# Optimization experiments

Measured on AMD Instinct MI355X. Metric: run time of the kernel, lower is better.

The kernel has to match this reference:

```python
import jax, jax.numpy as jnp
import numpy as np

# Module hyperparameters (match init_kwargs)
OUT_CHANNELS = 64
K = 19          # kernel_size
STRIDE = 5
PAD = 9
UPPER = 2.99
LOWER = -2.99

B = 64
L = 100000


def setup_inputs() -> dict:
    key = jax.random.key(0)
    k1, k2, k3 = jax.random.split(key, 3)
    x = jax.random.normal(k1, (B, 1, L), dtype=jnp.float32)
    # std_conv params: Conv1d(1, out_channels-2, K) -> weight (O-2, 1, K), bias (O-2,)
    W = jax.random.normal(k2, (OUT_CHANNELS - 2, 1, K), dtype=jnp.float32) * (1.0 / np.sqrt(K))
    b = jax.random.normal(k3, (OUT_CHANNELS - 2,), dtype=jnp.float32) * 0.01
    return {"x": x, "W": W, "b": b}


def _conv1d(x, w, stride, pad):
    # x: [B, Cin, L]; w: [Cout, Cin, K]
    return jax.lax.conv_general_dilated(
        x, w, window_strides=(stride,), padding=[(pad, pad)],
        dimension_numbers=("NCH", "OIH", "NCH"))


def reference(x, W, b):
    # Channel 0: windowed mean (non-differentiable / detached)
    mean_w = jnp.full((1, 1, K), 1.0 / K, dtype=x.dtype)
    mean_ch = jax.lax.stop_gradient(_conv1d(x, mean_w, STRIDE, PAD))  # [B,1,L_out]

    # Channel 1: threshold flag per window. any(x>UP) -> +1 ; elif any(x<LOWER) -> -1 ; else 0.
    # any(x > UP) over a window == (window max > UP); same for min. Zero-pad first
    # to match F.pad(..., value=0), then VALID reduce_window.
    xp = jnp.pad(x, ((0, 0), (0, 0), (PAD, PAD)))
    wmax = jax.lax.reduce_window(xp, -jnp.inf, jax.lax.max, (1, 1, K), (1, 1, STRIDE), "VALID")
    wmin = jax.lax.reduce_window(xp, jnp.inf, jax.lax.min, (1, 1, K), (1, 1, STRIDE), "VALID")
    thr_ch = jnp.where(wmax > UPPER, jnp.asarray(1.0, x.dtype),
                       jnp.where(wmin < LOWER, jnp.asarray(-1.0, x.dtype),
                                 jnp.asarray(0.0, x.dtype)))  # [B,1,L_out]
    thr_ch = jax.lax.stop_gradient(thr_ch)

    # Remaining channels: standard (differentiable) conv1d
    std_ch = _conv1d(x, W, STRIDE, PAD) + b[None, :, None]  # [B,O-2,L_out]

    return jnp.concatenate([mean_ch, thr_ch, std_ch], axis=1)  # [B, OUT_CHANNELS, L_out]
```

## Files before the change

### kernel.cpp

```cpp
#include <hip/hip_runtime.h>


#define BATCH       64
#define LIN         100000
#define LOUT        20000
#define KSZ         19
#define STRIDE_     5
#define PAD_        9
#define CSTD        62
#define UPPER_      2.99f
#define LOWER_      (-2.99f)

#define TPB         256
#define POS_PER_BLK 512
#define BPR         ((LOUT + POS_PER_BLK - 1) / POS_PER_BLK)
#define TILE_IN     ((POS_PER_BLK - 1) * STRIDE_ + KSZ)
#define WROW        20

__global__ __launch_bounds__(TPB)
void conv1d_mean_thr_kernel(const float* __restrict__ x,
                            const float* __restrict__ W,
                            const float* __restrict__ bias,
                            float* __restrict__ out)
{
    __shared__ float tile[TILE_IN];
    __shared__ float wsh[CSTD * WROW];
    __shared__ float bsh[CSTD];

    const int tid   = threadIdx.x;
    const int blk   = blockIdx.x;
    const int batch = blk / BPR;
    const int pblk  = blk - batch * BPR;
    const int p0    = pblk * POS_PER_BLK;
    const long tstart = (long)p0 * STRIDE_ - PAD_;

    const float* xrow = x + (size_t)batch * LIN;
    for (int i = tid; i < TILE_IN; i += TPB) {
        long g = tstart + i;
        tile[i] = (g >= 0 && g < LIN) ? xrow[g] : 0.0f;
    }
    for (int i = tid; i < CSTD * WROW; i += TPB) {
        int c = i / WROW, k = i - c * WROW;
        wsh[i] = (k < KSZ) ? W[c * KSZ + k] : 0.0f;
    }
    if (tid < CSTD) bsh[tid] = bias[tid];
    __syncthreads();

    float xv0[KSZ], xv1[KSZ];
    const int l0 = tid * STRIDE_;
    const int l1 = (tid + TPB) * STRIDE_;
#pragma unroll
    for (int k = 0; k < KSZ; ++k) {
        xv0[k] = tile[l0 + k];
        xv1[k] = tile[l1 + k];
    }

    const int pos0 = p0 + tid;
    const int pos1 = pos0 + TPB;
    const bool v0 = (pos0 < LOUT);
    const bool v1 = (pos1 < LOUT);
    float* orow = out + (size_t)batch * 64 * LOUT;

    float s0 = 0.f, s1 = 0.f;
    float mx0 = -INFINITY, mx1 = -INFINITY;
    float mn0 =  INFINITY, mn1 =  INFINITY;
#pragma unroll
    for (int k = 0; k < KSZ; ++k) {
        s0 += xv0[k]; mx0 = fmaxf(mx0, xv0[k]); mn0 = fminf(mn0, xv0[k]);
        s1 += xv1[k]; mx1 = fmaxf(mx1, xv1[k]); mn1 = fminf(mn1, xv1[k]);
    }
    const float inv_k = 1.0f / (float)KSZ;
    float thr0 = (mx0 > UPPER_) ? 1.0f : ((mn0 < LOWER_) ? -1.0f : 0.0f);
    float thr1 = (mx1 > UPPER_) ? 1.0f : ((mn1 < LOWER_) ? -1.0f : 0.0f);
    if (v0) { orow[pos0] = s0 * inv_k; orow[LOUT + pos0] = thr0; }
    if (v1) { orow[pos1] = s1 * inv_k; orow[LOUT + pos1] = thr1; }

    for (int c = 0; c < CSTD; ++c) {
        const float* wr = &wsh[c * WROW];
        float acc0 = 0.f, acc1 = 0.f;
#pragma unroll
        for (int k = 0; k < KSZ; ++k) {
            float wv = wr[k];
            acc0 = fmaf(xv0[k], wv, acc0);
            acc1 = fmaf(xv1[k], wv, acc1);
        }
        const float bv = bsh[c];
        size_t cbase = (size_t)(c + 2) * LOUT;
        if (v0) orow[cbase + pos0] = acc0 + bv;
        if (v1) orow[cbase + pos1] = acc1 + bv;
    }
}

extern "C" void kernel_launch(void* const* d_in, const int* in_sizes, int n_in,
                              void* d_out, int out_size, void* d_ws, size_t ws_size,
                              hipStream_t stream)
{
    const float* x    = (const float*)d_in[0];
    const float* W    = (const float*)d_in[1];
    const float* bias = (const float*)d_in[2];
    float* out        = (float*)d_out;

    dim3 grid(BATCH * BPR);
    dim3 block(TPB);
    conv1d_mean_thr_kernel<<<grid, block, 0, stream>>>(x, W, bias, out);
}
```

Before: 363.0 us.

## Compute four consecutive outputs per thread with vectorized LDS loads and float4 stores

Each thread now handles four adjacent output positions, so it needs one 36-float input window, loaded from shared memory as nine float4 reads, instead of two separate 19-float windows. Results go out as float4 stores per channel, which cuts the number of store instructions on a write-heavy output. Weights and bias are no longer staged in shared memory; they are read directly from global memory, where the wavefront-uniform addresses can use scalar loads. The trade-off is higher register pressure from the wider input window and a more rigid assumption that output rows are divisible by four and 16-byte aligned.

```diff
diff --git a/kernel.cpp b/kernel.cpp
--- a/kernel.cpp
+++ b/kernel.cpp
@@ -1,21 +1,22 @@
 #include <hip/hip_runtime.h>
 
 
-#define BATCH       64
-#define LIN         100000
-#define LOUT        20000
-#define KSZ         19
-#define STRIDE_     5
-#define PAD_        9
-#define CSTD        62
-#define UPPER_      2.99f
-#define LOWER_      (-2.99f)
+#define BATCH   64
+#define LIN     100000
+#define LOUT    20000
+#define KSZ     19
+#define STRIDE_ 5
+#define PAD_    9
+#define CSTD    62
+#define UPPER_  2.99f
+#define LOWER_  (-2.99f)
 
 #define TPB         256
-#define POS_PER_BLK 512
+#define PPT         4
+#define POS_PER_BLK (TPB * PPT)
 #define BPR         ((LOUT + POS_PER_BLK - 1) / POS_PER_BLK)
 #define TILE_IN     ((POS_PER_BLK - 1) * STRIDE_ + KSZ)
-#define WROW        20
+#define TILE_SZ     5136
 
 __global__ __launch_bounds__(TPB)
 void conv1d_mean_thr_kernel(const float* __restrict__ x,
@@ -23,9 +24,7 @@
                             const float* __restrict__ bias,
                             float* __restrict__ out)
 {
-    __shared__ float tile[TILE_IN];
-    __shared__ float wsh[CSTD * WROW];
-    __shared__ float bsh[CSTD];
+    __shared__ float tile[TILE_SZ];
 
     const int tid   = threadIdx.x;
     const int blk   = blockIdx.x;
@@ -35,59 +34,70 @@
     const long tstart = (long)p0 * STRIDE_ - PAD_;
 
     const float* xrow = x + (size_t)batch * LIN;
-    for (int i = tid; i < TILE_IN; i += TPB) {
+    for (int i = tid; i < TILE_SZ; i += TPB) {
         long g = tstart + i;
         tile[i] = (g >= 0 && g < LIN) ? xrow[g] : 0.0f;
     }
-    for (int i = tid; i < CSTD * WROW; i += TPB) {
-        int c = i / WROW, k = i - c * WROW;
-        wsh[i] = (k < KSZ) ? W[c * KSZ + k] : 0.0f;
-    }
-    if (tid < CSTD) bsh[tid] = bias[tid];
     __syncthreads();
 
-    float xv0[KSZ], xv1[KSZ];
-    const int l0 = tid * STRIDE_;
-    const int l1 = (tid + TPB) * STRIDE_;
+    float xw[36];
+    {
+        const float4* t4 = reinterpret_cast<const float4*>(tile);
 #pragma unroll
-    for (int k = 0; k < KSZ; ++k) {
-        xv0[k] = tile[l0 + k];
-        xv1[k] = tile[l1 + k];
+        for (int k = 0; k < 9; ++k) {
+            float4 v = t4[tid * 5 + k];
+            xw[4 * k + 0] = v.x;
+            xw[4 * k + 1] = v.y;
+            xw[4 * k + 2] = v.z;
+            xw[4 * k + 3] = v.w;
+        }
     }
 
-    const int pos0 = p0 + tid;
-    const int pos1 = pos0 + TPB;
-    const bool v0 = (pos0 < LOUT);
-    const bool v1 = (pos1 < LOUT);
-    float* orow = out + (size_t)batch * 64 * LOUT;
+    const int pos0   = p0 + tid * PPT;
+    const bool valid = (pos0 + PPT - 1) < LOUT;
+    float* outp = out + (size_t)batch * 64 * LOUT + pos0;
 
-    float s0 = 0.f, s1 = 0.f;
-    float mx0 = -INFINITY, mx1 = -INFINITY;
-    float mn0 =  INFINITY, mn1 =  INFINITY;
+    {
+        float mean[PPT], thr[PPT];
+        const float inv_k = 1.0f / (float)KSZ;
 #pragma unroll
-    for (int k = 0; k < KSZ; ++k) {
-        s0 += xv0[k]; mx0 = fmaxf(mx0, xv0[k]); mn0 = fminf(mn0, xv0[k]);
-        s1 += xv1[k]; mx1 = fmaxf(mx1, xv1[k]); mn1 = fminf(mn1, xv1[k]);
+        for (int j = 0; j < PPT; ++j) {
+            float s = 0.f, mx = -INFINITY, mn = INFINITY;
+#pragma unroll
+            for (int k = 0; k < KSZ; ++k) {
+                float v = xw[5 * j + k];
+                s += v; mx = fmaxf(mx, v); mn = fminf(mn, v);
+            }
+            mean[j] = s * inv_k;
+            thr[j]  = (mx > UPPER_) ? 1.0f : ((mn < LOWER_) ? -1.0f : 0.0f);
+        }
+        if (valid) {
+            *reinterpret_cast<float4*>(outp) =
+                make_float4(mean[0], mean[1], mean[2], mean[3]);
+            *reinterpret_cast<float4*>(outp + LOUT) =
+                make_float4(thr[0], thr[1], thr[2], thr[3]);
+        }
     }
-    const float inv_k = 1.0f / (float)KSZ;
-    float thr0 = (mx0 > UPPER_) ? 1.0f : ((mn0 < LOWER_) ? -1.0f : 0.0f);
-    float thr1 = (mx1 > UPPER_) ? 1.0f : ((mn1 < LOWER_) ? -1.0f : 0.0f);
-    if (v0) { orow[pos0] = s0 * inv_k; orow[LOUT + pos0] = thr0; }
-    if (v1) { orow[pos1] = s1 * inv_k; orow[LOUT + pos1] = thr1; }
 
     for (int c = 0; c < CSTD; ++c) {
-        const float* wr = &wsh[c * WROW];
-        float acc0 = 0.f, acc1 = 0.f;
+        float w[KSZ];
 #pragma unroll
-        for (int k = 0; k < KSZ; ++k) {
-            float wv = wr[k];
-            acc0 = fmaf(xv0[k], wv, acc0);
-            acc1 = fmaf(xv1[k], wv, acc1);
+        for (int k = 0; k < KSZ; ++k) w[k] = W[c * KSZ + k];
+        const float bv = bias[c];
+
+        float acc[PPT];
+#pragma unroll
+        for (int j = 0; j < PPT; ++j) {
+            float a = 0.f;
+#pragma unroll
+            for (int k = 0; k < KSZ; ++k)
+                a = fmaf(xw[5 * j + k], w[k], a);
+            acc[j] = a + bv;
         }
-        const float bv = bsh[c];
-        size_t cbase = (size_t)(c + 2) * LOUT;
-        if (v0) orow[cbase + pos0] = acc0 + bv;
-        if (v1) orow[cbase + pos1] = acc1 + bv;
+        if (valid) {
+            *reinterpret_cast<float4*>(outp + (size_t)(c + 2) * LOUT) =
+                make_float4(acc[0], acc[1], acc[2], acc[3]);
+        }
     }
 }
 
```

Result: no change. 364.6 us (+0.5%).
